# Kernel tuning notes

Measured on AMD Instinct MI355X. Metric: run time of the kernel, lower is better.

## Reference

```python
import jax, jax.numpy as jnp
import numpy as np
from jax import lax

INF = jnp.float32(1e30)  # large finite stand-in for np.inf (keeps vjp NaN-free)


def setup_inputs() -> dict:
    key = jax.random.key(0)
    k1, k2 = jax.random.split(key)
    M = 2048
    N = 2048
    source = jax.random.normal(k1, (M,), dtype=jnp.float32)
    target = jax.random.normal(k2, (N,), dtype=jnp.float32)
    return {"source": source, "target": target}


def _dtw_sq(source, target):
    # DP over rows: row i holds DTW[i, 0..n]. Only two rows live at a time.
    n = target.shape[0]
    row0 = jnp.concatenate([jnp.zeros((1,), jnp.float32),
                            jnp.full((n,), INF, jnp.float32)])  # DTW[0, :]

    def row_step(prev_row, s_i):
        dists = (s_i - target) ** 2  # [n], cost of cell (i, j)

        def cell(left, xs):
            d, up_left, up = xs  # DTW[i-1,j-1], DTW[i-1,j]; left = DTW[i,j-1]
            cur = d + jnp.minimum(jnp.minimum(up, left), up_left)
            return cur, cur

        _, row_vals = lax.scan(cell, INF, (dists, prev_row[:-1], prev_row[1:]))
        new_row = jnp.concatenate([jnp.full((1,), INF, jnp.float32), row_vals])
        return new_row, None

    final_row, _ = lax.scan(row_step, row0, source)
    return final_row[-1]  # DTW[m, n]


def reference(source, target):
    loss_sq = _dtw_sq(source, target)
    return jnp.sqrt(loss_sq)[None]  # shape (1,), matching torch.Tensor([..])
```

## Files before the change

### kernel.cpp

```cpp
#include <hip/hip_runtime.h>
#include <math.h>


#define MM 2048
#define NN 2048
#define BR 4
#define BC 8
#define NT 256
#define NB (MM / BR)
#define KK 16
#define DELTA (63 + KK)
#define MAXSKEW (63 + 3 * DELTA)
#define NITER (NB + MAXSKEW)
#define NSP ((NITER + KK - 1) / KK)
#define RING (2 * KK)
#define INFV 1e30f

__launch_bounds__(NT, 1)
__global__ void dtw_kernel(const float* __restrict__ src,
                           const float* __restrict__ tgt,
                           float* __restrict__ out)
{
    __shared__ float4 s_src4[NB];
    __shared__ float4 mbox[3][RING];

    const int tid  = threadIdx.x;
    const int wv   = tid >> 6;
    const int ln   = tid & 63;
    const int skew = ln + wv * DELTA;

    const float4* s4 = (const float4*)src;
    for (int i = tid; i < NB; i += NT) s_src4[i] = s4[i];

    float tg[BC];
    #pragma unroll
    for (int k = 0; k < BC; ++k) tg[k] = tgt[tid * BC + k];

    float cur[BC];
    #pragma unroll
    for (int k = 0; k < BC; ++k) cur[k] = INFV;

    float corner = (tid == 0) ? 0.0f : INFV;
    float4 rcp = make_float4(INFV, INFV, INFV, INFV);

    __syncthreads();

    for (int sp = 0; sp < NSP; ++sp) {
        #pragma unroll 1
        for (int it = 0; it < KK; ++it) {
            const int n = sp * KK + it;

            float lc0 = __shfl_up(rcp.x, 1);
            float lc1 = __shfl_up(rcp.y, 1);
            float lc2 = __shfl_up(rcp.z, 1);
            float lc3 = __shfl_up(rcp.w, 1);
            if (ln == 0) {
                if (wv == 0) {
                    lc0 = lc1 = lc2 = lc3 = INFV;
                } else {
                    float4 m = mbox[wv - 1][(n - KK) & (RING - 1)];
                    lc0 = m.x; lc1 = m.y; lc2 = m.z; lc3 = m.w;
                }
            }

            const int bi = n - skew;
            if (0 <= bi && bi < NB) {
                float4 sv = s_src4[bi];
                float srow[BR] = {sv.x, sv.y, sv.z, sv.w};
                float lcx[BR]  = {lc0, lc1, lc2, lc3};

                float dg[BR], lv[BR];
                dg[0] = corner;
                lv[0] = lcx[0];
                #pragma unroll
                for (int r = 1; r < BR; ++r) { dg[r] = lcx[r - 1]; lv[r] = lcx[r]; }

                #pragma unroll
                for (int s = 0; s < BR + BC - 1; ++s) {
                    #pragma unroll
                    for (int r = 0; r < BR; ++r) {
                        const int k = s - r;
                        if (0 <= k && k < BC) {
                            float up = cur[k];
                            float m  = fminf(fminf(up, lv[r]), dg[r]);
                            float d  = srow[r] - tg[k];
                            float v  = fmaf(d, d, m);
                            dg[r] = up;
                            lv[r] = v;
                            cur[k] = v;
                        }
                    }
                }

                corner = lcx[BR - 1];
                rcp = make_float4(lv[0], lv[1], lv[2], lv[3]);
                if (ln == 63 && wv < 3)
                    mbox[wv][n & (RING - 1)] = rcp;
            }
        }
        __syncthreads();
    }

    if (tid == NT - 1) out[0] = sqrtf(cur[BC - 1]);
}

extern "C" void kernel_launch(void* const* d_in, const int* in_sizes, int n_in,
                              void* d_out, int out_size, void* d_ws, size_t ws_size,
                              hipStream_t stream)
{
    (void)in_sizes; (void)n_in; (void)out_size; (void)d_ws; (void)ws_size;
    const float* source = (const float*)d_in[0];
    const float* target = (const float*)d_in[1];
    float* out = (float*)d_out;
    dtw_kernel<<<1, NT, 0, stream>>>(source, target, out);
}
```

Measured before the change: 262.8 us.

## Enlarge per-thread DTW tile to 8x8 and prefetch next-step inputs

Each thread's block grows from 4 to 8 source rows, which halves the number of wavefront iterations while doubling the cells computed per iteration. The synchronization interval KK is reduced and the wave skew DELTA adjusted to match. The source-row load and the left-column shuffle and mailbox reads for the next iteration are moved to the end of the current iteration, so they overlap with the dependency chain instead of sitting at its head. In exchange, each iteration has a longer dependency chain, more shuffles, and more block-wide syncs, and register pressure rises.

```diff
diff --git a/kernel.cpp b/kernel.cpp
--- a/kernel.cpp
+++ b/kernel.cpp
@@ -4,12 +4,12 @@
 
 #define MM 2048
 #define NN 2048
-#define BR 4
+#define BR 8
 #define BC 8
 #define NT 256
 #define NB (MM / BR)
-#define KK 16
-#define DELTA (63 + KK)
+#define KK 8
+#define DELTA (63 + KK + 1)
 #define MAXSKEW (63 + 3 * DELTA)
 #define NITER (NB + MAXSKEW)
 #define NSP ((NITER + KK - 1) / KK)
@@ -21,8 +21,8 @@
                            const float* __restrict__ tgt,
                            float* __restrict__ out)
 {
-    __shared__ float4 s_src4[NB];
-    __shared__ float4 mbox[3][RING];
+    __shared__ float4 s_src4[MM / 4];
+    __shared__ float4 mbox[3][RING][2];
 
     const int tid  = threadIdx.x;
     const int wv   = tid >> 6;
@@ -30,7 +30,7 @@
     const int skew = ln + wv * DELTA;
 
     const float4* s4 = (const float4*)src;
-    for (int i = tid; i < NB; i += NT) s_src4[i] = s4[i];
+    for (int i = tid; i < MM / 4; i += NT) s_src4[i] = s4[i];
 
     float tg[BC];
     #pragma unroll
@@ -41,37 +41,36 @@
     for (int k = 0; k < BC; ++k) cur[k] = INFV;
 
     float corner = (tid == 0) ? 0.0f : INFV;
-    float4 rcp = make_float4(INFV, INFV, INFV, INFV);
+
+    float rcp[BR];
+    #pragma unroll
+    for (int r = 0; r < BR; ++r) rcp[r] = INFV;
 
     __syncthreads();
+
+    float lc[BR], psrow[BR];
+    {
+        #pragma unroll
+        for (int r = 0; r < BR; ++r) lc[r] = INFV;
+        int bin = 0 - skew; if (bin < 0) bin = 0;
+        float4 a = s_src4[2 * bin], b = s_src4[2 * bin + 1];
+        psrow[0] = a.x; psrow[1] = a.y; psrow[2] = a.z; psrow[3] = a.w;
+        psrow[4] = b.x; psrow[5] = b.y; psrow[6] = b.z; psrow[7] = b.w;
+    }
 
     for (int sp = 0; sp < NSP; ++sp) {
         #pragma unroll 1
         for (int it = 0; it < KK; ++it) {
-            const int n = sp * KK + it;
+            const int n  = sp * KK + it;
+            const int bi = n - skew;
 
-            float lc0 = __shfl_up(rcp.x, 1);
-            float lc1 = __shfl_up(rcp.y, 1);
-            float lc2 = __shfl_up(rcp.z, 1);
-            float lc3 = __shfl_up(rcp.w, 1);
-            if (ln == 0) {
-                if (wv == 0) {
-                    lc0 = lc1 = lc2 = lc3 = INFV;
-                } else {
-                    float4 m = mbox[wv - 1][(n - KK) & (RING - 1)];
-                    lc0 = m.x; lc1 = m.y; lc2 = m.z; lc3 = m.w;
-                }
-            }
-
-            const int bi = n - skew;
             if (0 <= bi && bi < NB) {
-                float4 sv = s_src4[bi];
-                float srow[BR] = {sv.x, sv.y, sv.z, sv.w};
-                float lcx[BR]  = {lc0, lc1, lc2, lc3};
+                float srow[BR], lcx[BR];
+                #pragma unroll
+                for (int r = 0; r < BR; ++r) { srow[r] = psrow[r]; lcx[r] = lc[r]; }
 
                 float dg[BR], lv[BR];
-                dg[0] = corner;
-                lv[0] = lcx[0];
+                dg[0] = corner; lv[0] = lcx[0];
                 #pragma unroll
                 for (int r = 1; r < BR; ++r) { dg[r] = lcx[r - 1]; lv[r] = lcx[r]; }
 
@@ -85,17 +84,43 @@
                             float m  = fminf(fminf(up, lv[r]), dg[r]);
                             float d  = srow[r] - tg[k];
                             float v  = fmaf(d, d, m);
-                            dg[r] = up;
-                            lv[r] = v;
-                            cur[k] = v;
+                            dg[r] = up; lv[r] = v; cur[k] = v;
                         }
                     }
                 }
 
                 corner = lcx[BR - 1];
-                rcp = make_float4(lv[0], lv[1], lv[2], lv[3]);
-                if (ln == 63 && wv < 3)
-                    mbox[wv][n & (RING - 1)] = rcp;
+                #pragma unroll
+                for (int r = 0; r < BR; ++r) rcp[r] = lv[r];
+                if (ln == 63 && wv < 3) {
+                    const int sl = n & (RING - 1);
+                    mbox[wv][sl][0] = make_float4(rcp[0], rcp[1], rcp[2], rcp[3]);
+                    mbox[wv][sl][1] = make_float4(rcp[4], rcp[5], rcp[6], rcp[7]);
+                }
+            }
+
+            {
+                int bin = n + 1 - skew;
+                if (bin < 0) bin = 0;
+                if (bin > NB - 1) bin = NB - 1;
+                float4 a = s_src4[2 * bin], b = s_src4[2 * bin + 1];
+                psrow[0] = a.x; psrow[1] = a.y; psrow[2] = a.z; psrow[3] = a.w;
+                psrow[4] = b.x; psrow[5] = b.y; psrow[6] = b.z; psrow[7] = b.w;
+
+                #pragma unroll
+                for (int r = 0; r < BR; ++r) lc[r] = __shfl_up(rcp[r], 1);
+                if (ln == 0) {
+                    if (wv == 0) {
+                        #pragma unroll
+                        for (int r = 0; r < BR; ++r) lc[r] = INFV;
+                    } else {
+                        const int sl = (int)((unsigned)(n - KK) & (RING - 1));
+                        float4 m0 = mbox[wv - 1][sl][0];
+                        float4 m1 = mbox[wv - 1][sl][1];
+                        lc[0] = m0.x; lc[1] = m0.y; lc[2] = m0.z; lc[3] = m0.w;
+                        lc[4] = m1.x; lc[5] = m1.y; lc[6] = m1.z; lc[7] = m1.w;
+                    }
+                }
             }
         }
         __syncthreads();
```

Measured after the change: 288.4 us. 9.8% more time.
